# Kernel optimization log

Hardware: AMD Instinct MI355X
Metric: run time of the kernel (lower is better)

Reference implementation:

```python
import jax, jax.numpy as jnp
import numpy as np

CDIM = 32
SCALES = (1, 16, 64, 256, 1024, 4096)  # last entry == T
INV_TEMP = 100.0
ENT_W = 0.1
COMMIT_W = 0.2
Q_SCALE = 1.0 / float(np.sqrt(CDIM))


def _interp_area(x, pt):
    # x: [B, T, C] -> [B, pt, C]; T divisible by pt so 'area' == block mean
    B, T, C = x.shape
    return x.reshape(B, pt, T // pt, C).mean(axis=2)


def _interp_linear(x, T):
    # x: [B, pt, C] -> [B, T, C]; mode='linear', align_corners=False
    pt = x.shape[1]
    pos = (jnp.arange(T, dtype=jnp.float32) + 0.5) * (pt / T) - 0.5
    pos = jnp.clip(pos, 0.0, pt - 1.0)
    lo = jnp.floor(pos).astype(jnp.int32)
    hi = jnp.minimum(lo + 1, pt - 1)
    w = (pos - lo.astype(jnp.float32))[None, :, None]
    return x[:, lo] * (1.0 - w) + x[:, hi] * w


def _bsq(f):
    # L2 normalize (torch F.normalize: clamp_min on norm)
    f = f / jnp.maximum(jnp.linalg.norm(f, axis=-1, keepdims=True), 1e-12)
    # sign quantize with STE
    zhat = jnp.where(f > 0, Q_SCALE, -Q_SCALE).astype(f.dtype)
    quantized = f + jax.lax.stop_gradient(zhat - f)
    # soft entropy loss
    p = jax.nn.sigmoid(-4.0 * f * (INV_TEMP / float(np.sqrt(CDIM))))
    prob = jnp.stack([p, 1.0 - p], axis=-1)  # [B, T, C, 2]
    ent = lambda c: -(c * jnp.log(c + 1e-8)).sum(axis=-1)
    per_sample_entropy = ent(prob).sum(axis=-1).mean()
    avg_prob = prob.mean(axis=(0, 1))  # [C, 2]
    cb_entropy = ent(avg_prob).sum()
    entropy_penalty = (per_sample_entropy - cb_entropy) / INV_TEMP
    commit = ((jax.lax.stop_gradient(quantized) - f) ** 2).sum(axis=-1).mean()
    aux = entropy_penalty * ENT_W + commit * COMMIT_W
    bits = (quantized > 0).astype(jnp.int32)
    return quantized, bits, aux


def setup_inputs() -> dict:
    key = jax.random.key(0)
    B, T, C = 128, SCALES[-1], CDIM
    return {"f_BTC": jax.random.normal(key, (B, T, C), dtype=jnp.float32)}


def reference(f_BTC):
    B, T, C = f_BTC.shape
    quantized_out = jnp.zeros_like(f_BTC)
    residual = f_BTC
    losses, bit_list = [], []
    for pt in SCALES:
        interp_res = _interp_area(residual, pt) if pt != T else residual
        q, bits, loss = _bsq(interp_res)
        q = _interp_linear(q, T) if pt != T else q
        residual = residual - jax.lax.stop_gradient(q)
        quantized_out = quantized_out + q
        bit_list.append(bits)
        losses.append(loss)
    all_losses = jnp.stack(losses, axis=-1)       # [num_scales]
    all_bits = jnp.concatenate(bit_list, axis=1)  # [B, sum(SCALES), C]
    return quantized_out, all_bits, all_losses
```

## Files before the change

### kernel.cpp

```cpp
#include <hip/hip_runtime.h>
#include <hip/hip_bf16.h>
#include <cstddef>
#include <cstdint>

#define NB 128
#define NT 4096
#define NC 32
#define BITROWS 5457
#define QV_ROWS 1361
#define QOUT_ELEMS (NB*NT*NC)
#define BITS_ELEMS (NB*BITROWS*NC)

#define ACC_OFF  22298624
#define S16_OFF  22302720

__device__ __constant__ float kQSC = 0.17677669529663687f;
__device__ __constant__ float kSIG = 17.67766952966369f;

__device__ __forceinline__ float interp_slice(const float* __restrict__ q, int P, int base, int t, int c) {
  float pos = ((float)t + 0.5f) * ((float)P * (1.0f / 4096.0f)) - 0.5f;
  pos = fminf(fmaxf(pos, 0.0f), (float)(P - 1));
  const int lo = (int)pos;
  const int hi = min(lo + 1, P - 1);
  const float w = pos - (float)lo;
  const float a = __fmul_rn(q[(lo - base) * NC + c], 1.0f - w);
  const float b = __fmul_rn(q[(hi - base) * NC + c], w);
  return __fadd_rn(a, b);
}

__device__ __forceinline__ void process_elem(
    float msum, float invn, int b, int rowOff, int j, int c,
    float* qlsRow, float* __restrict__ qvG, float* __restrict__ bitsG,
    float& entA, float& comA, float& pA)
{
  const float m = msum * invn;
  float ss = m * m;
  #pragma unroll
  for (int mk = 16; mk; mk >>= 1) ss += __shfl_xor(ss, mk, 32);
  const float den = fmaxf(sqrtf(ss), 1e-12f);
  const float fn = m / den;
  const bool bit = fn > 0.0f;
  const float zh = bit ? kQSC : -kQSC;
  const float qvv = fn + (zh - fn);
  if (qlsRow) qlsRow[c] = qvv;
  if (qvG) qvG[(size_t)b * (QV_ROWS * NC) + (size_t)(rowOff + j) * NC + c] = qvv;
  bitsG[(size_t)b * (BITROWS * NC) + (size_t)(rowOff + j) * NC + c] = bit ? 1.0f : 0.0f;
  const float arg = (-4.0f * fn) * kSIG;
  const float p = 1.0f / (1.0f + __expf(-arg));
  const float ent = -(p * __logf(p + 1e-8f) + (1.0f - p) * __logf((1.0f - p) + 1e-8f));
  const float d = qvv - fn;
  entA += ent; comA += d * d; pA += p;
}

__device__ __forceinline__ float quant_silent(float msum, float invn) {
  const float m = msum * invn;
  float ss = m * m;
  #pragma unroll
  for (int mk = 16; mk; mk >>= 1) ss += __shfl_xor(ss, mk, 32);
  const float den = fmaxf(sqrtf(ss), 1e-12f);
  const float fn = m / den;
  const float zh = (fn > 0.0f) ? kQSC : -kQSC;
  return fn + (zh - fn);
}

__device__ __forceinline__ void reduce_losses(
    int sIdx, float entA, float comA, float pA, int tid, int nWaves,
    double* __restrict__ acc, float* redE, float* redC, float* redP)
{
  float e = entA, cm = comA;
  #pragma unroll
  for (int mk = 32; mk; mk >>= 1) { e += __shfl_xor(e, mk, 64); cm += __shfl_xor(cm, mk, 64); }
  const float p = pA + __shfl_xor(pA, 32, 64);
  const int w = tid >> 6, lane = tid & 63;
  if (lane == 0) { redE[w] = e; redC[w] = cm; }
  if (lane < 32) redP[w * 32 + lane] = p;
  __syncthreads();
  if (tid == 0) {
    double te = 0.0, tc = 0.0;
    for (int i = 0; i < nWaves; ++i) { te += (double)redE[i]; tc += (double)redC[i]; }
    atomicAdd(&acc[sIdx], te);
    atomicAdd(&acc[6 + sIdx], tc);
  }
  if (tid < 32) {
    float tp = 0.0f;
    for (int i = 0; i < nWaves; ++i) tp += redP[i * 32 + tid];
    atomicAdd(&acc[12 + sIdx * 32 + tid], (double)tp);
  }
  __syncthreads();
}

__global__ __launch_bounds__(256) void k_sum16(const float* __restrict__ f, float* __restrict__ S16) {
  const int idx = blockIdx.x * 256 + threadIdx.x;
  if (idx >= NB * 256 * NC) return;
  const int c = idx & 31;
  const int j = (idx >> 5) & 255;
  const int b = idx >> 13;
  const float* p = f + (size_t)b * (NT * NC) + (size_t)j * 16 * NC + c;
  float s = 0.0f;
  #pragma unroll
  for (int k = 0; k < 16; ++k) s += p[k * NC];
  S16[idx] = s;
}

__global__ __launch_bounds__(1024) void k_s0(
    const float* __restrict__ S16g, float* __restrict__ qv,
    float* __restrict__ bitsOut, double* __restrict__ acc)
{
  __shared__ float red[1024];
  __shared__ float redE[16], redC[16], redP[16 * 32];
  const int b = blockIdx.x, tid = threadIdx.x, c = tid & 31;
  const float* __restrict__ sb = S16g + (size_t)b * 8192;
  {
    const int g = tid >> 5;
    float part = 0.0f;
    #pragma unroll
    for (int j = 0; j < 8; ++j) part += sb[(size_t)(g * 8 + j) * NC + c];
    red[tid] = part;
  }
  __syncthreads();
  float entA = 0.0f, comA = 0.0f, pA = 0.0f;
  if (tid < 32) {
    float msum = 0.0f;
    for (int g = 0; g < 32; ++g) msum += red[g * 32 + tid];
    process_elem(msum, 1.0f / 4096.0f, b, 0, 0, tid, nullptr, qv, bitsOut, entA, comA, pA);
  }
  reduce_losses(0, entA, comA, pA, tid, 16, acc, redE, redC, redP);
}

__global__ __launch_bounds__(256) void k_fused(
    const float* __restrict__ f, const float* __restrict__ S16g,
    const float* __restrict__ qv, float* __restrict__ qout,
    float* __restrict__ bitsOut, double* __restrict__ acc)
{
  __shared__ float S[48 * NC];
  __shared__ float q1s[3 * NC];
  __shared__ float q2s[6 * NC];
  __shared__ float q3s[18 * NC];
  __shared__ float ql4[66 * NC];
  __shared__ float redE[4], redC[4], redP[4 * 32];
  const int b = blockIdx.x >> 4, seg = blockIdx.x & 15;
  const int tid = threadIdx.x, c = tid & 31, rloc = tid >> 5;
  const float* __restrict__ fb = f + (size_t)b * (NT * NC);
  const float* __restrict__ sb = S16g + (size_t)b * 8192;
  const int b1 = seg - 1, b2 = 4 * seg - 1, b3 = 16 * seg - 1, b4 = 64 * seg - 1;
  const int srow0 = 16 * seg - 16;
  const float q0v = qv[(size_t)b * (QV_ROWS * NC) + c];

  for (int e = tid; e < 48 * NC; e += 256) {
    const int rw = min(max(srow0 + (e >> 5), 0), 255);
    S[e] = sb[(size_t)rw * NC + (e & 31)] - 16.0f * q0v;
  }
  __syncthreads();

  float ent = 0.0f, com = 0.0f, pp = 0.0f;

  if (tid < 3 * NC) {
    const int r = tid >> 5, j = b1 + r;
    if (j >= 0 && j < 16) {
      float msum = 0.0f;
      for (int jj = 0; jj < 16; ++jj) msum += S[(j * 16 + jj - srow0) * NC + c];
      if (r == 1)
        process_elem(msum, 1.0f / 256.0f, b, 1, j, c, &q1s[r * NC], nullptr, bitsOut, ent, com, pp);
      else
        q1s[r * NC + c] = quant_silent(msum, 1.0f / 256.0f);
    }
  }
  reduce_losses(1, ent, com, pp, tid, 4, acc, redE, redC, redP);

  for (int e = tid; e < 24 * NC; e += 256) {
    const int g = 16 * seg - 4 + (e >> 5);
    if (g >= 0 && g < 256) {
      float cs = 0.0f;
      #pragma unroll
      for (int k = 0; k < 16; ++k) cs += interp_slice(q1s, 16, b1, g * 16 + k, c);
      S[(g - srow0) * NC + c] -= cs;
    }
  }
  __syncthreads();

  ent = com = pp = 0.0f;
  if (tid < 6 * NC) {
    const int r = tid >> 5, j2 = b2 + r;
    if (j2 >= 0 && j2 < 64) {
      float msum = 0.0f;
      #pragma unroll
      for (int jj = 0; jj < 4; ++jj) msum += S[(j2 * 4 + jj - srow0) * NC + c];
      if (r >= 1 && r <= 4)
        process_elem(msum, 1.0f / 64.0f, b, 17, j2, c, &q2s[r * NC], nullptr, bitsOut, ent, com, pp);
      else
        q2s[r * NC + c] = quant_silent(msum, 1.0f / 64.0f);
    }
  }
  reduce_losses(2, ent, com, pp, tid, 4, acc, redE, redC, redP);

  for (int e = tid; e < 18 * NC; e += 256) {
    const int g = 16 * seg - 1 + (e >> 5);
    if (g >= 0 && g < 256) {
      float cs = 0.0f;
      #pragma unroll
      for (int k = 0; k < 16; ++k) cs += interp_slice(q2s, 64, b2, g * 16 + k, c);
      S[(g - srow0) * NC + c] -= cs;
    }
  }
  __syncthreads();

  ent = com = pp = 0.0f;
  for (int e = tid; e < 18 * NC; e += 256) {
    const int r = e >> 5, g = b3 + r;
    if (g >= 0 && g < 256) {
      const float ms = S[(g - srow0) * NC + c];
      if (r >= 1 && r <= 16)
        process_elem(ms, 1.0f / 16.0f, b, 81, g, c, &q3s[r * NC], nullptr, bitsOut, ent, com, pp);
      else
        q3s[r * NC + c] = quant_silent(ms, 1.0f / 16.0f);
    }
  }
  reduce_losses(3, ent, com, pp, tid, 4, acc, redE, redC, redP);

  float entA4 = 0.0f, comA4 = 0.0f, pA4 = 0.0f;
  float entB = 0.0f, comB = 0.0f, pB = 0.0f;

  auto do_A = [&](int p, float rc[4], float qc[4]) {
    const int i = seg * 64 + p * 8 + rloc;
    const float* fp = fb + (size_t)i * 4 * NC + c;
    float msum = 0.0f;
    #pragma unroll
    for (int k = 0; k < 4; ++k) {
      const int t = i * 4 + k;
      const float q0 = q0v;
      const float q1 = interp_slice(q1s, 16,  b1, t, c);
      const float q2 = interp_slice(q2s, 64,  b2, t, c);
      const float q3 = interp_slice(q3s, 256, b3, t, c);
      float r = fp[k * NC];
      r -= q0; r -= q1; r -= q2; r -= q3;
      float qs = q0; qs += q1; qs += q2; qs += q3;
      rc[k] = r; qc[k] = qs;
      msum += r;
    }
    process_elem(msum, 0.25f, b, 337, i, c,
                 &ql4[(size_t)(i - b4) * NC], nullptr, bitsOut, entA4, comA4, pA4);
  };

  auto do_halo = [&](int hr) {
    const float* fp = fb + (size_t)hr * 4 * NC + c;
    float msum = 0.0f;
    #pragma unroll
    for (int k = 0; k < 4; ++k) {
      const int t = hr * 4 + k;
      float r = fp[k * NC];
      r -= q0v;
      r -= interp_slice(q1s, 16,  b1, t, c);
      r -= interp_slice(q2s, 64,  b2, t, c);
      r -= interp_slice(q3s, 256, b3, t, c);
      msum += r;
    }
    ql4[(size_t)(hr - b4) * NC + c] = quant_silent(msum, 0.25f);
  };

  auto do_B = [&](int p, const float rc[4], const float qc[4]) {
    const int i = seg * 64 + p * 8 + rloc;
    #pragma unroll
    for (int k = 0; k < 4; ++k) {
      const int t = i * 4 + k;
      const float q4 = interp_slice(ql4, 1024, b4, t, c);
      float r = rc[k];
      r -= q4;
      float qs = qc[k];
      qs += q4;
      float ss = r * r;
      #pragma unroll
      for (int mk = 16; mk; mk >>= 1) ss += __shfl_xor(ss, mk, 32);
      const float den = fmaxf(sqrtf(ss), 1e-12f);
      const float fn = r / den;
      const bool bit = fn > 0.0f;
      const float zh = bit ? kQSC : -kQSC;
      const float qvv = fn + (zh - fn);
      qout[(size_t)b * (NT * NC) + (size_t)t * NC + c] = qs + qvv;
      bitsOut[(size_t)b * (BITROWS * NC) + (size_t)(1361 + t) * NC + c] = bit ? 1.0f : 0.0f;
      const float arg = (-4.0f * fn) * kSIG;
      const float p2 = 1.0f / (1.0f + __expf(-arg));
      entB += -(p2 * __logf(p2 + 1e-8f) + (1.0f - p2) * __logf((1.0f - p2) + 1e-8f));
      const float d = qvv - fn;
      comB += d * d;
      pB += p2;
    }
  };

  float rAp[4], qsAp[4];
  float rAc[4], qsAc[4];

  do_A(0, rAp, qsAp);
  if (rloc == 0 && seg > 0) do_halo(64 * seg - 1);

  for (int p = 1; p < 8; ++p) {
    do_A(p, rAc, qsAc);
    __syncthreads();
    do_B(p - 1, rAp, qsAp);
    #pragma unroll
    for (int k = 0; k < 4; ++k) { rAp[k] = rAc[k]; qsAp[k] = qsAc[k]; }
  }
  if (rloc == 1 && seg < 15) do_halo(64 * seg + 64);
  __syncthreads();
  do_B(7, rAp, qsAp);

  reduce_losses(4, entA4, comA4, pA4, tid, 4, acc, redE, redC, redP);
  reduce_losses(5, entB, comB, pB, tid, 4, acc, redE, redC, redP);
}

__global__ void k_losses(const double* __restrict__ acc, float* __restrict__ out) {
  const int s = threadIdx.x;
  if (s >= 6) return;
  const int pts[6] = {1, 16, 64, 256, 1024, 4096};
  const double n = 128.0 * (double)pts[s];
  const double pse = acc[s] / n;
  const double commit = acc[6 + s] / n;
  double cbe = 0.0;
  for (int c = 0; c < 32; ++c) {
    const double ap = acc[12 + s * 32 + c] / n;
    cbe += -(ap * log(ap + 1e-8) + (1.0 - ap) * log((1.0 - ap) + 1e-8));
  }
  const double pen = (pse - cbe) / 100.0;
  out[s] = (float)(pen * 0.1 + commit * 0.2);
}

extern "C" void kernel_launch(void* const* d_in, const int* in_sizes, int n_in,
                              void* d_out, int out_size, void* d_ws, size_t ws_size,
                              hipStream_t stream) {
  const float* f = (const float*)d_in[0];
  float* qout = (float*)d_out;
  float* bitsOut = qout + QOUT_ELEMS;
  float* lossesOut = qout + (QOUT_ELEMS + BITS_ELEMS);
  float* qv = (float*)d_ws;
  double* acc = (double*)((char*)d_ws + ACC_OFF);
  float* S16 = (float*)((char*)d_ws + S16_OFF);

  hipMemsetAsync(acc, 0, 204 * sizeof(double), stream);
  k_sum16<<<4096, 256, 0, stream>>>(f, S16);
  k_s0<<<NB, 1024, 0, stream>>>(S16, qv, bitsOut, acc);
  k_fused<<<NB * 16, 256, 0, stream>>>(f, S16, qv, qout, bitsOut, acc);
  k_losses<<<1, 64, 0, stream>>>(acc, lossesOut);
}
```

Baseline: 390.5 us.

## Split coarse scales into separate kernel to cut redundant halo recomputation

Moves the scale-1/2/3 quantization (16, 64, 256 points) out of the per-segment fused kernel into a new kernel with 4 blocks of 1024 threads per batch. That kernel writes the quantized values to the workspace. The fine-scale kernel then reads these precomputed rows instead of recomputing coarse scales and halos in every one of 16 segments. This removes duplicated work and serialized syncs from the bandwidth-bound fine kernel, at the cost of one extra launch and a small global round trip.

Result: faster. 320.6 us (-17.9%).

```diff
diff --git a/kernel.cpp b/kernel.cpp
--- a/kernel.cpp
+++ b/kernel.cpp
@@ -127,95 +127,116 @@
   reduce_losses(0, entA, comA, pA, tid, 16, acc, redE, redC, redP);
 }
 
-__global__ __launch_bounds__(256) void k_fused(
-    const float* __restrict__ f, const float* __restrict__ S16g,
-    const float* __restrict__ qv, float* __restrict__ qout,
-    float* __restrict__ bitsOut, double* __restrict__ acc)
-{
-  __shared__ float S[48 * NC];
-  __shared__ float q1s[3 * NC];
-  __shared__ float q2s[6 * NC];
-  __shared__ float q3s[18 * NC];
+__global__ __launch_bounds__(1024) void k_coarse4(
+    const float* __restrict__ S16g,
+    float* __restrict__ qv, float* __restrict__ bitsOut, double* __restrict__ acc)
+{
+  __shared__ float S[96 * NC];
+  __shared__ float q1s[6 * NC];
+  __shared__ float q2s[18 * NC];
+  __shared__ float redE[16], redC[16], redP[16 * 32];
+  const int b = blockIdx.x >> 2, seg = blockIdx.x & 3;
+  const int tid = threadIdx.x, c = tid & 31;
+  const int s0r = 64 * seg - 16;
+  const int base1 = 4 * seg - 1, base2 = 16 * seg - 1;
+  const float* __restrict__ sb = S16g + (size_t)b * 8192;
+  const float* __restrict__ qb = qv + (size_t)b * (QV_ROWS * NC);
+
+  const float corr = 16.0f * qb[c];
+  for (int e = tid; e < 96 * NC; e += 1024) {
+    const int rw = min(max(s0r + (e >> 5), 0), 255);
+    S[e] = sb[(size_t)rw * NC + (e & 31)] - corr;
+  }
+  __syncthreads();
+
+  float ent, com, pp;
+
+  ent = com = pp = 0.0f;
+  if (tid < 6 * NC) {
+    const int r = tid >> 5, j = base1 + r;
+    if (j >= 0 && j < 16) {
+      float msum = 0.0f;
+      for (int jj = 0; jj < 16; ++jj) msum += S[(j * 16 + jj - s0r) * NC + c];
+      if (r >= 1 && r <= 4)
+        process_elem(msum, 1.0f / 256.0f, b, 1, j, c, &q1s[r * NC], qv, bitsOut, ent, com, pp);
+      else
+        q1s[r * NC + c] = quant_silent(msum, 1.0f / 256.0f);
+    }
+  }
+  reduce_losses(1, ent, com, pp, tid, 16, acc, redE, redC, redP);
+
+  for (int e = tid; e < 72 * NC; e += 1024) {
+    const int g = 64 * seg - 4 + (e >> 5);
+    if (g >= 0 && g < 256) {
+      float cs = 0.0f;
+      #pragma unroll
+      for (int k = 0; k < 16; ++k) cs += interp_slice(q1s, 16, base1, g * 16 + k, c);
+      S[(g - s0r) * NC + c] -= cs;
+    }
+  }
+  __syncthreads();
+
+  ent = com = pp = 0.0f;
+  if (tid < 18 * NC) {
+    const int r = tid >> 5, j2 = base2 + r;
+    if (j2 >= 0 && j2 < 64) {
+      float msum = 0.0f;
+      #pragma unroll
+      for (int jj = 0; jj < 4; ++jj) msum += S[(j2 * 4 + jj - s0r) * NC + c];
+      if (r >= 1 && r <= 16)
+        process_elem(msum, 1.0f / 64.0f, b, 17, j2, c, &q2s[r * NC], qv, bitsOut, ent, com, pp);
+      else
+        q2s[r * NC + c] = quant_silent(msum, 1.0f / 64.0f);
+    }
+  }
+  reduce_losses(2, ent, com, pp, tid, 16, acc, redE, redC, redP);
+
+  for (int e = tid; e < 64 * NC; e += 1024) {
+    const int g = 64 * seg + (e >> 5);
+    float cs = 0.0f;
+    #pragma unroll
+    for (int k = 0; k < 16; ++k) cs += interp_slice(q2s, 64, base2, g * 16 + k, c);
+    S[(g - s0r) * NC + c] -= cs;
+  }
+  __syncthreads();
+
+  ent = com = pp = 0.0f;
+  for (int out = tid; out < 64 * NC; out += 1024) {
+    const int g = 64 * seg + (out >> 5);
+    process_elem(S[(g - s0r) * NC + c], 1.0f / 16.0f, b, 81, g, c, nullptr, qv, bitsOut, ent, com, pp);
+  }
+  reduce_losses(3, ent, com, pp, tid, 16, acc, redE, redC, redP);
+}
+
+__global__ __launch_bounds__(256) void k_s45(
+    const float* __restrict__ f, const float* __restrict__ qv,
+    float* __restrict__ qout, float* __restrict__ bitsOut, double* __restrict__ acc)
+{
+  __shared__ float ql0[NC];
+  __shared__ float ql1[3 * NC];
+  __shared__ float ql2[6 * NC];
+  __shared__ float ql3[18 * NC];
   __shared__ float ql4[66 * NC];
   __shared__ float redE[4], redC[4], redP[4 * 32];
   const int b = blockIdx.x >> 4, seg = blockIdx.x & 15;
   const int tid = threadIdx.x, c = tid & 31, rloc = tid >> 5;
+  const float* __restrict__ qb = qv + (size_t)b * (QV_ROWS * NC);
   const float* __restrict__ fb = f + (size_t)b * (NT * NC);
-  const float* __restrict__ sb = S16g + (size_t)b * 8192;
   const int b1 = seg - 1, b2 = 4 * seg - 1, b3 = 16 * seg - 1, b4 = 64 * seg - 1;
-  const int srow0 = 16 * seg - 16;
-  const float q0v = qv[(size_t)b * (QV_ROWS * NC) + c];
-
-  for (int e = tid; e < 48 * NC; e += 256) {
-    const int rw = min(max(srow0 + (e >> 5), 0), 255);
-    S[e] = sb[(size_t)rw * NC + (e & 31)] - 16.0f * q0v;
-  }
-  __syncthreads();
-
-  float ent = 0.0f, com = 0.0f, pp = 0.0f;
-
-  if (tid < 3 * NC) {
-    const int r = tid >> 5, j = b1 + r;
-    if (j >= 0 && j < 16) {
-      float msum = 0.0f;
-      for (int jj = 0; jj < 16; ++jj) msum += S[(j * 16 + jj - srow0) * NC + c];
-      if (r == 1)
-        process_elem(msum, 1.0f / 256.0f, b, 1, j, c, &q1s[r * NC], nullptr, bitsOut, ent, com, pp);
-      else
-        q1s[r * NC + c] = quant_silent(msum, 1.0f / 256.0f);
-    }
-  }
-  reduce_losses(1, ent, com, pp, tid, 4, acc, redE, redC, redP);
-
-  for (int e = tid; e < 24 * NC; e += 256) {
-    const int g = 16 * seg - 4 + (e >> 5);
-    if (g >= 0 && g < 256) {
-      float cs = 0.0f;
-      #pragma unroll
-      for (int k = 0; k < 16; ++k) cs += interp_slice(q1s, 16, b1, g * 16 + k, c);
-      S[(g - srow0) * NC + c] -= cs;
-    }
-  }
-  __syncthreads();
-
-  ent = com = pp = 0.0f;
-  if (tid < 6 * NC) {
-    const int r = tid >> 5, j2 = b2 + r;
-    if (j2 >= 0 && j2 < 64) {
-      float msum = 0.0f;
-      #pragma unroll
-      for (int jj = 0; jj < 4; ++jj) msum += S[(j2 * 4 + jj - srow0) * NC + c];
-      if (r >= 1 && r <= 4)
-        process_elem(msum, 1.0f / 64.0f, b, 17, j2, c, &q2s[r * NC], nullptr, bitsOut, ent, com, pp);
-      else
-        q2s[r * NC + c] = quant_silent(msum, 1.0f / 64.0f);
-    }
-  }
-  reduce_losses(2, ent, com, pp, tid, 4, acc, redE, redC, redP);
-
+  if (tid < NC) ql0[tid] = qb[tid];
+  for (int e = tid; e < 3 * NC; e += 256) {
+    const int r = min(max(b1 + (e >> 5), 0), 15);
+    ql1[e] = qb[(1 + r) * NC + (e & 31)];
+  }
+  for (int e = tid; e < 6 * NC; e += 256) {
+    const int r = min(max(b2 + (e >> 5), 0), 63);
+    ql2[e] = qb[(17 + r) * NC + (e & 31)];
+  }
   for (int e = tid; e < 18 * NC; e += 256) {
-    const int g = 16 * seg - 1 + (e >> 5);
-    if (g >= 0 && g < 256) {
-      float cs = 0.0f;
-      #pragma unroll
-      for (int k = 0; k < 16; ++k) cs += interp_slice(q2s, 64, b2, g * 16 + k, c);
-      S[(g - srow0) * NC + c] -= cs;
-    }
-  }
-  __syncthreads();
-
-  ent = com = pp = 0.0f;
-  for (int e = tid; e < 18 * NC; e += 256) {
-    const int r = e >> 5, g = b3 + r;
-    if (g >= 0 && g < 256) {
-      const float ms = S[(g - srow0) * NC + c];
-      if (r >= 1 && r <= 16)
-        process_elem(ms, 1.0f / 16.0f, b, 81, g, c, &q3s[r * NC], nullptr, bitsOut, ent, com, pp);
-      else
-        q3s[r * NC + c] = quant_silent(ms, 1.0f / 16.0f);
-    }
-  }
-  reduce_losses(3, ent, com, pp, tid, 4, acc, redE, redC, redP);
+    const int r = min(max(b3 + (e >> 5), 0), 255);
+    ql3[e] = qb[(81 + r) * NC + (e & 31)];
+  }
+  __syncthreads();
 
   float entA4 = 0.0f, comA4 = 0.0f, pA4 = 0.0f;
   float entB = 0.0f, comB = 0.0f, pB = 0.0f;
@@ -227,10 +248,10 @@
     #pragma unroll
     for (int k = 0; k < 4; ++k) {
       const int t = i * 4 + k;
-      const float q0 = q0v;
-      const float q1 = interp_slice(q1s, 16,  b1, t, c);
-      const float q2 = interp_slice(q2s, 64,  b2, t, c);
-      const float q3 = interp_slice(q3s, 256, b3, t, c);
+      const float q0 = ql0[c];
+      const float q1 = interp_slice(ql1, 16,  b1, t, c);
+      const float q2 = interp_slice(ql2, 64,  b2, t, c);
+      const float q3 = interp_slice(ql3, 256, b3, t, c);
       float r = fp[k * NC];
       r -= q0; r -= q1; r -= q2; r -= q3;
       float qs = q0; qs += q1; qs += q2; qs += q3;
@@ -248,10 +269,10 @@
     for (int k = 0; k < 4; ++k) {
       const int t = hr * 4 + k;
       float r = fp[k * NC];
-      r -= q0v;
-      r -= interp_slice(q1s, 16,  b1, t, c);
-      r -= interp_slice(q2s, 64,  b2, t, c);
-      r -= interp_slice(q3s, 256, b3, t, c);
+      r -= ql0[c];
+      r -= interp_slice(ql1, 16,  b1, t, c);
+      r -= interp_slice(ql2, 64,  b2, t, c);
+      r -= interp_slice(ql3, 256, b3, t, c);
       msum += r;
     }
     ql4[(size_t)(hr - b4) * NC + c] = quant_silent(msum, 0.25f);
@@ -337,6 +358,7 @@
   hipMemsetAsync(acc, 0, 204 * sizeof(double), stream);
   k_sum16<<<4096, 256, 0, stream>>>(f, S16);
   k_s0<<<NB, 1024, 0, stream>>>(S16, qv, bitsOut, acc);
-  k_fused<<<NB * 16, 256, 0, stream>>>(f, S16, qv, qout, bitsOut, acc);
+  k_coarse4<<<NB * 4, 1024, 0, stream>>>(S16, qv, bitsOut, acc);
+  k_s45<<<NB * 16, 256, 0, stream>>>(f, qv, qout, bitsOut, acc);
   k_losses<<<1, 64, 0, stream>>>(acc, lossesOut);
 }
```
